# Optimization experiments

Measured on AMD Instinct MI355X. Metric: run time of the kernel, lower is better.

Reference implementation:

```python
import jax, jax.numpy as jnp
import numpy as np

N_NODES = 100000
N_EDGES = 3200000
FEATURE = 128
HIDDEN = 128
N_LAYERS = 3


def _glorot(key, fan_in, fan_out):
    lim = np.sqrt(6.0 / (fan_in + fan_out)).astype(np.float32)
    return jax.random.uniform(key, (fan_in, fan_out), jnp.float32, -lim, lim)


def setup_inputs() -> dict:
    key = jax.random.key(0)
    ks = jax.random.split(key, 8)
    x = jax.random.normal(ks[0], (N_NODES, FEATURE), jnp.float32)
    edge_index = jax.random.randint(ks[1], (2, N_EDGES), 0, N_NODES, jnp.int64)
    W0 = _glorot(ks[2], FEATURE, HIDDEN)
    W1 = _glorot(ks[3], HIDDEN, HIDDEN)
    W2 = _glorot(ks[4], HIDDEN, HIDDEN)
    b0 = jnp.zeros((HIDDEN,), jnp.float32)
    b1 = jnp.zeros((HIDDEN,), jnp.float32)
    b2 = jnp.zeros((HIDDEN,), jnp.float32)
    return {"x": x, "edge_index": edge_index,
            "W0": W0, "b0": b0, "W1": W1, "b1": b1, "W2": W2, "b2": b2}


def _gcn_conv(x, W, b, src, dst, n):
    # PyG GCNConv: linear -> add self loops -> sym-norm aggregate -> +bias
    h = x @ W  # [N, H]
    loop = jnp.arange(n)
    s = jnp.concatenate([src, loop])  # sources incl. self loops
    d = jnp.concatenate([dst, loop])  # targets incl. self loops
    deg = jax.ops.segment_sum(jnp.ones_like(d, dtype=h.dtype), d, num_segments=n)
    dinv = jnp.where(deg > 0, jax.lax.rsqrt(jnp.maximum(deg, 1.0)), 0.0)
    norm = dinv[s] * dinv[d]  # [E+N]
    out = jax.ops.segment_sum(h[s] * norm[:, None], d, num_segments=n)
    return out + b


def reference(x, edge_index, W0, b0, W1, b1, W2, b2):
    # forward of GCN: (GCNConv -> relu -> dropout[eval=no-op]) x layer
    src, dst = edge_index[0], edge_index[1]
    n = x.shape[0]
    for W, b in ((W0, b0), (W1, b1), (W2, b2)):
        x = jax.nn.relu(_gcn_conv(x, W, b, src, dst, n))
    return x
```

## Files before the change

### kernel.cpp

```cpp
#include <hip/hip_runtime.h>
#include <hip/hip_fp16.h>

#define N_NODES 100000
#define N_EDGES 3200000
#define NBUCKETS 391
#define CHUNK 12500

typedef __attribute__((ext_vector_type(8))) short sh8;
typedef __attribute__((ext_vector_type(4))) float fl4;

__device__ inline void split_bf16(float x, short& hi, short& lo) {
    unsigned u = __float_as_uint(x);
    unsigned r = u + 0x7FFFu + ((u >> 16) & 1u);
    hi = (short)(r >> 16);
    float hif = __uint_as_float(r & 0xFFFF0000u);
    float lof = x - hif;
    unsigned u2 = __float_as_uint(lof);
    lo = (short)((u2 + 0x7FFFu + ((u2 >> 16) & 1u)) >> 16);
}


__global__ __launch_bounds__(512) void k_bzero(int* __restrict__ bucket_cnt) {
    int t = threadIdx.x;
    if (t < NBUCKETS) bucket_cnt[t] = 0;
}

__global__ __launch_bounds__(256) void k_bhist(const int* __restrict__ ei_dst,
                                               int* __restrict__ bucket_cnt) {
    __shared__ int h[NBUCKETS];
    int t = threadIdx.x;
    for (int i = t; i < NBUCKETS; i += 256) h[i] = 0;
    __syncthreads();
    int base = blockIdx.x * CHUNK;
    for (int i = t; i < CHUNK; i += 256)
        atomicAdd(&h[ei_dst[base + i] >> 8], 1);
    __syncthreads();
    for (int i = t; i < NBUCKETS; i += 256)
        if (h[i]) atomicAdd(&bucket_cnt[i], h[i]);
}

__global__ __launch_bounds__(512) void k_bscan(const int* __restrict__ bucket_cnt,
                                               int* __restrict__ bucket_base,
                                               int* __restrict__ bucket_fill) {
    __shared__ int s[512];
    int t = threadIdx.x;
    int v = (t < NBUCKETS) ? bucket_cnt[t] : 0;
    s[t] = v;
    __syncthreads();
    for (int off = 1; off < 512; off <<= 1) {
        int x = (t >= off) ? s[t - off] : 0;
        __syncthreads();
        s[t] += x;
        __syncthreads();
    }
    int ex = s[t] - v;
    if (t < NBUCKETS) { bucket_base[t] = ex; bucket_fill[t] = ex; }
    if (t == NBUCKETS - 1) bucket_base[NBUCKETS] = s[t];
}

__global__ __launch_bounds__(256) void k_bscatter(const int* __restrict__ ei,
                                                  int* __restrict__ bucket_fill,
                                                  unsigned* __restrict__ bpairs) {
    __shared__ int h[NBUCKETS];
    __shared__ int basep[NBUCKETS];
    int t = threadIdx.x;
    const int* dstp = ei + N_EDGES;
    int base = blockIdx.x * CHUNK;

    for (int i = t; i < NBUCKETS; i += 256) h[i] = 0;
    __syncthreads();
    for (int i = t; i < CHUNK; i += 256)
        atomicAdd(&h[dstp[base + i] >> 8], 1);
    __syncthreads();
    for (int i = t; i < NBUCKETS; i += 256) {
        int c = h[i];
        basep[i] = c ? atomicAdd(&bucket_fill[i], c) : 0;
    }
    __syncthreads();
    for (int i = t; i < NBUCKETS; i += 256) h[i] = 0;
    __syncthreads();
    for (int i = t; i < CHUNK; i += 256) {
        int d = dstp[base + i];
        int s = ei[base + i];
        int b = d >> 8;
        int r = atomicAdd(&h[b], 1);
        bpairs[basep[b] + r] = (unsigned)s | ((unsigned)(d & 255) << 17);
    }
}

__global__ __launch_bounds__(256) void k_bbuild(const unsigned* __restrict__ bpairs,
                                                const int* __restrict__ bucket_base,
                                                int* __restrict__ row_ptr,
                                                int* __restrict__ cnt,
                                                float* __restrict__ dinv,
                                                int* __restrict__ csr_src) {
    __shared__ int h[256];
    __shared__ int sc[256];
    int b = blockIdx.x;
    int t = threadIdx.x;
    int e0 = bucket_base[b], e1 = bucket_base[b + 1];

    h[t] = 0;
    __syncthreads();
    for (int i = e0 + t; i < e1; i += 256)
        atomicAdd(&h[bpairs[i] >> 17], 1);
    __syncthreads();
    int v = h[t];
    sc[t] = v;
    __syncthreads();
    for (int off = 1; off < 256; off <<= 1) {
        int x = (t >= off) ? sc[t - off] : 0;
        __syncthreads();
        sc[t] += x;
        __syncthreads();
    }
    int ex = sc[t] - v;
    int node = b * 256 + t;
    if (node < N_NODES) {
        cnt[node] = v;
        dinv[node] = rsqrtf((float)(v + 1));
        row_ptr[node] = e0 + ex;
    }
    __syncthreads();
    h[t] = e0 + ex;
    __syncthreads();
    for (int i = e0 + t; i < e1; i += 256) {
        unsigned p = bpairs[i];
        int pos = atomicAdd(&h[p >> 17], 1);
        csr_src[pos] = (int)(p & 0x1FFFFu);
    }
}


__global__ __launch_bounds__(256) void k_wprep(const float* __restrict__ W0,
                                               const float* __restrict__ W1,
                                               const float* __restrict__ W2,
                                               short* __restrict__ fhi,
                                               short* __restrict__ flo) {
    int idx = blockIdx.x * 256 + threadIdx.x;
    int l = idx >> 14, e = idx & 16383;
    const float* W = (l == 0) ? W0 : (l == 1) ? W1 : W2;
    float w = W[e];
    int k = e >> 7, n = e & 127;
    int ks = k >> 5, q = (k >> 3) & 3, j = k & 7;
    int c = n >> 4, n16 = n & 15;
    int lane = q * 16 + n16;
    int dst = ((l * 32 + ks * 8 + c) * 64 + lane) * 8 + j;
    short hi, lo;
    split_bf16(w, hi, lo);
    fhi[dst] = hi;
    flo[dst] = lo;
}


__global__ __launch_bounds__(256) void k_gemm_mfma(const float* __restrict__ X,
                                                   const short* __restrict__ fhi,
                                                   const short* __restrict__ flo,
                                                   const float* __restrict__ dinv,
                                                   __half* __restrict__ H16,
                                                   int layer) {
    int t = threadIdx.x;
    int wave = t >> 6, lane = t & 63;
    int q = lane >> 4, n16 = lane & 15;
    int row_base = blockIdx.x * 128 + wave * 32;

    const sh8* __restrict__ BH = (const sh8*)(fhi + layer * 16384);
    const sh8* __restrict__ BL = (const sh8*)(flo + layer * 16384);

    fl4 acc[2][8];
#pragma unroll
    for (int r = 0; r < 2; ++r)
#pragma unroll
        for (int c = 0; c < 8; ++c) acc[r][c] = (fl4){0.f, 0.f, 0.f, 0.f};

    long long arow[2];
    {
        int r0 = row_base + n16;       if (r0 > N_NODES - 1) r0 = N_NODES - 1;
        int r1 = row_base + 16 + n16;  if (r1 > N_NODES - 1) r1 = N_NODES - 1;
        arow[0] = r0; arow[1] = r1;
    }

#pragma unroll
    for (int ks = 0; ks < 4; ++ks) {
        sh8 ah[2], al[2];
#pragma unroll
        for (int r = 0; r < 2; ++r) {
            const float* px = X + arow[r] * 128 + ks * 32 + q * 8;
            float4 x0 = *(const float4*)px;
            float4 x1 = *(const float4*)(px + 4);
            float xs[8] = {x0.x, x0.y, x0.z, x0.w, x1.x, x1.y, x1.z, x1.w};
#pragma unroll
            for (int j = 0; j < 8; ++j) {
                short h, l;
                split_bf16(xs[j], h, l);
                ah[r][j] = h;
                al[r][j] = l;
            }
        }
#pragma unroll
        for (int c = 0; c < 8; ++c) {
            sh8 bh = BH[(ks * 8 + c) * 64 + lane];
            sh8 bl = BL[(ks * 8 + c) * 64 + lane];
#pragma unroll
            for (int r = 0; r < 2; ++r) {
                acc[r][c] = __builtin_amdgcn_mfma_f32_16x16x32_bf16(ah[r], bh, acc[r][c], 0, 0, 0);
                acc[r][c] = __builtin_amdgcn_mfma_f32_16x16x32_bf16(al[r], bh, acc[r][c], 0, 0, 0);
                acc[r][c] = __builtin_amdgcn_mfma_f32_16x16x32_bf16(ah[r], bl, acc[r][c], 0, 0, 0);
            }
        }
    }

#pragma unroll
    for (int r = 0; r < 2; ++r)
#pragma unroll
        for (int reg = 0; reg < 4; ++reg) {
            int grow = row_base + r * 16 + q * 4 + reg;
            if (grow < N_NODES) {
                float sc = dinv[grow];
                __half* dst = H16 + (long long)grow * 128 + n16;
#pragma unroll
                for (int c = 0; c < 8; ++c)
                    dst[c * 16] = __float2half(acc[r][c][reg] * sc);
            }
        }
}


__global__ __launch_bounds__(256) void k_gather(const __half2* __restrict__ H2,
                                                const int* __restrict__ csr_src,
                                                const int* __restrict__ row_ptr,
                                                const int* __restrict__ cnt,
                                                const float* __restrict__ dinv,
                                                const float* __restrict__ b,
                                                float* __restrict__ out) {
    int node = blockIdx.x * 4 + (threadIdx.x >> 6);
    int lane = threadIdx.x & 63;
    if (node >= N_NODES) return;

    int start = row_ptr[node];
    int n = cnt[node];

    float2 self_ = __half22float2(H2[node * 64 + lane]);
    float accx = self_.x, accy = self_.y;

    int j = 0;
    for (; j + 8 <= n; j += 8) {
        int s[8];
#pragma unroll
        for (int u = 0; u < 8; ++u) s[u] = csr_src[start + j + u];
        float2 h[8];
#pragma unroll
        for (int u = 0; u < 8; ++u) h[u] = __half22float2(H2[s[u] * 64 + lane]);
#pragma unroll
        for (int u = 0; u < 8; ++u) { accx += h[u].x; accy += h[u].y; }
    }
    for (; j < n; ++j) {
        float2 h = __half22float2(H2[csr_src[start + j] * 64 + lane]);
        accx += h.x; accy += h.y;
    }

    float dd = dinv[node];
    float2 bb = ((const float2*)b)[lane];
    float2 v;
    v.x = fmaxf(fmaf(accx, dd, bb.x), 0.0f);
    v.y = fmaxf(fmaf(accy, dd, bb.y), 0.0f);
    ((float2*)out)[node * 64 + lane] = v;
}


extern "C" void kernel_launch(void* const* d_in, const int* in_sizes, int n_in,
                              void* d_out, int out_size, void* d_ws, size_t ws_size,
                              hipStream_t stream) {
    const float* x  = (const float*)d_in[0];
    const int*   ei = (const int*)d_in[1];
    const float* Wm[3] = {(const float*)d_in[2], (const float*)d_in[4], (const float*)d_in[6]};
    const float* bv[3] = {(const float*)d_in[3], (const float*)d_in[5], (const float*)d_in[7]};
    float* out = (float*)d_out;

    char* w = (char*)d_ws;
    int*      row_ptr     = (int*)(w + 0);
    int*      cnt         = (int*)(w + 400384);
    float*    dinv        = (float*)(w + 800768);
    int*      bucket_cnt  = (int*)(w + 1201152);
    int*      bucket_base = (int*)(w + 1203200);
    int*      bucket_fill = (int*)(w + 1205248);
    unsigned* bpairs      = (unsigned*)(w + 1207296);
    int*      csr_src     = (int*)(w + 14007808);
    short*    fragHi      = (short*)(w + 26808320);
    short*    fragLo      = (short*)(w + 26906624);
    __half*   H16         = (__half*)(w + 27004928);

    k_bzero<<<1, 512, 0, stream>>>(bucket_cnt);
    k_bhist<<<256, 256, 0, stream>>>(ei + N_EDGES, bucket_cnt);
    k_bscan<<<1, 512, 0, stream>>>(bucket_cnt, bucket_base, bucket_fill);
    k_bscatter<<<256, 256, 0, stream>>>(ei, bucket_fill, bpairs);
    k_bbuild<<<NBUCKETS, 256, 0, stream>>>(bpairs, bucket_base, row_ptr, cnt, dinv, csr_src);
    k_wprep<<<192, 256, 0, stream>>>(Wm[0], Wm[1], Wm[2], fragHi, fragLo);

    const float* xin = x;
    for (int l = 0; l < 3; ++l) {
        k_gemm_mfma<<<(N_NODES + 127) / 128, 256, 0, stream>>>(xin, fragHi, fragLo,
                                                               dinv, H16, l);
        k_gather<<<(N_NODES + 3) / 4, 256, 0, stream>>>((const __half2*)H16, csr_src,
                                                        row_ptr, cnt, dinv, bv[l], out);
        xin = out;
    }
}
```

Measured before the change: 650.6 us.

## Stage split-bf16 weights in LDS and prefetch all A rows upfront in GEMM

The MFMA GEMM kernel now copies the layer's hi/lo bf16 weight fragments (64KB) into shared memory once per block and reads them from LDS instead of global memory. All of a thread's X row data is loaded up front and split to bf16 before the MFMA loop, so global loads overlap the weight staging. This adds a barrier and high LDS use, which limits blocks per CU (launch bounds request 2). Register pressure also rises from holding all A fragments.

```diff
diff --git a/kernel.cpp b/kernel.cpp
--- a/kernel.cpp
+++ b/kernel.cpp
@@ -153,62 +153,85 @@
 }
 
 
-__global__ __launch_bounds__(256) void k_gemm_mfma(const float* __restrict__ X,
-                                                   const short* __restrict__ fhi,
-                                                   const short* __restrict__ flo,
-                                                   const float* __restrict__ dinv,
-                                                   __half* __restrict__ H16,
-                                                   int layer) {
+__global__ __launch_bounds__(256, 2) void k_gemm_mfma(const float* __restrict__ X,
+                                                      const short* __restrict__ fhi,
+                                                      const short* __restrict__ flo,
+                                                      const float* __restrict__ dinv,
+                                                      __half* __restrict__ H16,
+                                                      int layer) {
+    __shared__ short Bh[16384];
+    __shared__ short Bl[16384];
+
     int t = threadIdx.x;
     int wave = t >> 6, lane = t & 63;
     int q = lane >> 4, n16 = lane & 15;
     int row_base = blockIdx.x * 128 + wave * 32;
 
-    const sh8* __restrict__ BH = (const sh8*)(fhi + layer * 16384);
-    const sh8* __restrict__ BL = (const sh8*)(flo + layer * 16384);
-
-    fl4 acc[2][8];
+    int r0 = row_base + n16;       if (r0 > N_NODES - 1) r0 = N_NODES - 1;
+    int r1 = row_base + 16 + n16;  if (r1 > N_NODES - 1) r1 = N_NODES - 1;
+    const float* p0 = X + (long long)r0 * 128 + q * 8;
+    const float* p1 = X + (long long)r1 * 128 + q * 8;
+    float4 a[2][4][2];
+#pragma unroll
+    for (int ks = 0; ks < 4; ++ks) {
+        a[0][ks][0] = *(const float4*)(p0 + ks * 32);
+        a[0][ks][1] = *(const float4*)(p0 + ks * 32 + 4);
+        a[1][ks][0] = *(const float4*)(p1 + ks * 32);
+        a[1][ks][1] = *(const float4*)(p1 + ks * 32 + 4);
+    }
+
+    {
+        const float4* sh_ = (const float4*)(fhi + layer * 16384);
+        const float4* sl_ = (const float4*)(flo + layer * 16384);
+        float4* dh = (float4*)Bh;
+        float4* dl = (float4*)Bl;
+#pragma unroll
+        for (int i = 0; i < 8; ++i) {
+            dh[t + i * 256] = sh_[t + i * 256];
+            dl[t + i * 256] = sl_[t + i * 256];
+        }
+    }
+
+    sh8 ah[2][4], al[2][4];
 #pragma unroll
     for (int r = 0; r < 2; ++r)
 #pragma unroll
-        for (int c = 0; c < 8; ++c) acc[r][c] = (fl4){0.f, 0.f, 0.f, 0.f};
-
-    long long arow[2];
-    {
-        int r0 = row_base + n16;       if (r0 > N_NODES - 1) r0 = N_NODES - 1;
-        int r1 = row_base + 16 + n16;  if (r1 > N_NODES - 1) r1 = N_NODES - 1;
-        arow[0] = r0; arow[1] = r1;
-    }
-
-#pragma unroll
-    for (int ks = 0; ks < 4; ++ks) {
-        sh8 ah[2], al[2];
-#pragma unroll
-        for (int r = 0; r < 2; ++r) {
-            const float* px = X + arow[r] * 128 + ks * 32 + q * 8;
-            float4 x0 = *(const float4*)px;
-            float4 x1 = *(const float4*)(px + 4);
-            float xs[8] = {x0.x, x0.y, x0.z, x0.w, x1.x, x1.y, x1.z, x1.w};
+        for (int ks = 0; ks < 4; ++ks) {
+            float xs[8];
+            xs[0] = a[r][ks][0].x; xs[1] = a[r][ks][0].y;
+            xs[2] = a[r][ks][0].z; xs[3] = a[r][ks][0].w;
+            xs[4] = a[r][ks][1].x; xs[5] = a[r][ks][1].y;
+            xs[6] = a[r][ks][1].z; xs[7] = a[r][ks][1].w;
 #pragma unroll
             for (int j = 0; j < 8; ++j) {
                 short h, l;
                 split_bf16(xs[j], h, l);
-                ah[r][j] = h;
-                al[r][j] = l;
+                ah[r][ks][j] = h;
+                al[r][ks][j] = l;
             }
         }
+
+    fl4 acc[2][8];
+#pragma unroll
+    for (int r = 0; r < 2; ++r)
+#pragma unroll
+        for (int c = 0; c < 8; ++c) acc[r][c] = (fl4){0.f, 0.f, 0.f, 0.f};
+
+    __syncthreads();
+
+#pragma unroll
+    for (int ks = 0; ks < 4; ++ks)
 #pragma unroll
         for (int c = 0; c < 8; ++c) {
-            sh8 bh = BH[(ks * 8 + c) * 64 + lane];
-            sh8 bl = BL[(ks * 8 + c) * 64 + lane];
+            sh8 bh = *(const sh8*)&Bh[((ks * 8 + c) * 64 + lane) * 8];
+            sh8 bl = *(const sh8*)&Bl[((ks * 8 + c) * 64 + lane) * 8];
 #pragma unroll
             for (int r = 0; r < 2; ++r) {
-                acc[r][c] = __builtin_amdgcn_mfma_f32_16x16x32_bf16(ah[r], bh, acc[r][c], 0, 0, 0);
-                acc[r][c] = __builtin_amdgcn_mfma_f32_16x16x32_bf16(al[r], bh, acc[r][c], 0, 0, 0);
-                acc[r][c] = __builtin_amdgcn_mfma_f32_16x16x32_bf16(ah[r], bl, acc[r][c], 0, 0, 0);
+                acc[r][c] = __builtin_amdgcn_mfma_f32_16x16x32_bf16(ah[r][ks], bh, acc[r][c], 0, 0, 0);
+                acc[r][c] = __builtin_amdgcn_mfma_f32_16x16x32_bf16(al[r][ks], bh, acc[r][c], 0, 0, 0);
+                acc[r][c] = __builtin_amdgcn_mfma_f32_16x16x32_bf16(ah[r][ks], bl, acc[r][c], 0, 0, 0);
             }
         }
-    }
 
 #pragma unroll
     for (int r = 0; r < 2; ++r)
```

Result: faster. 625.8 us (-3.8%).

## Shrink GEMM tile to 16 rows per wave, preload inputs, double CSR-build chunk count

Applied to the files above, without the earlier changes.

The MFMA GEMM now has each wave handle a single 16-row tile instead of two. It preloads all four K-slices of X up front and batches the B-fragment loads per K-step. Launch bounds request 3 blocks per SM, and the grid grows to 1563 blocks, aiming for more waves in flight and better latency hiding at the cost of reusing each B fragment across fewer rows. The CSR bucket histogram and scatter now use 512 chunks of 6250 edges for more parallelism. The gather kernel makes the wave index uniform via readfirstlane.

```diff
diff --git a/kernel.cpp b/kernel.cpp
--- a/kernel.cpp
+++ b/kernel.cpp
@@ -4,7 +4,8 @@
 #define N_NODES 100000
 #define N_EDGES 3200000
 #define NBUCKETS 391
-#define CHUNK 12500
+#define NCHUNKB 512
+#define CHUNK 6250
 
 typedef __attribute__((ext_vector_type(8))) short sh8;
 typedef __attribute__((ext_vector_type(4))) float fl4;
@@ -153,76 +154,76 @@
 }
 
 
-__global__ __launch_bounds__(256) void k_gemm_mfma(const float* __restrict__ X,
-                                                   const short* __restrict__ fhi,
-                                                   const short* __restrict__ flo,
-                                                   const float* __restrict__ dinv,
-                                                   __half* __restrict__ H16,
-                                                   int layer) {
+__global__ __launch_bounds__(256, 3) void k_gemm_mfma(const float* __restrict__ X,
+                                                      const short* __restrict__ fhi,
+                                                      const short* __restrict__ flo,
+                                                      const float* __restrict__ dinv,
+                                                      __half* __restrict__ H16) {
     int t = threadIdx.x;
     int wave = t >> 6, lane = t & 63;
     int q = lane >> 4, n16 = lane & 15;
-    int row_base = blockIdx.x * 128 + wave * 32;
-
-    const sh8* __restrict__ BH = (const sh8*)(fhi + layer * 16384);
-    const sh8* __restrict__ BL = (const sh8*)(flo + layer * 16384);
-
-    fl4 acc[2][8];
-#pragma unroll
-    for (int r = 0; r < 2; ++r)
-#pragma unroll
-        for (int c = 0; c < 8; ++c) acc[r][c] = (fl4){0.f, 0.f, 0.f, 0.f};
-
-    long long arow[2];
-    {
-        int r0 = row_base + n16;       if (r0 > N_NODES - 1) r0 = N_NODES - 1;
-        int r1 = row_base + 16 + n16;  if (r1 > N_NODES - 1) r1 = N_NODES - 1;
-        arow[0] = r0; arow[1] = r1;
-    }
-
+    int tile = blockIdx.x * 4 + wave;
+    int row_base = tile * 16;
+
+    int r0 = row_base + n16;
+    if (r0 > N_NODES - 1) r0 = N_NODES - 1;
+    const float* p0 = X + (long long)r0 * 128 + q * 8;
+    float4 a[4][2];
 #pragma unroll
     for (int ks = 0; ks < 4; ++ks) {
-        sh8 ah[2], al[2];
-#pragma unroll
-        for (int r = 0; r < 2; ++r) {
-            const float* px = X + arow[r] * 128 + ks * 32 + q * 8;
-            float4 x0 = *(const float4*)px;
-            float4 x1 = *(const float4*)(px + 4);
-            float xs[8] = {x0.x, x0.y, x0.z, x0.w, x1.x, x1.y, x1.z, x1.w};
-#pragma unroll
-            for (int j = 0; j < 8; ++j) {
-                short h, l;
-                split_bf16(xs[j], h, l);
-                ah[r][j] = h;
-                al[r][j] = l;
-            }
+        a[ks][0] = *(const float4*)(p0 + ks * 32);
+        a[ks][1] = *(const float4*)(p0 + ks * 32 + 4);
+    }
+
+    sh8 ah[4], al[4];
+#pragma unroll
+    for (int ks = 0; ks < 4; ++ks) {
+        float xs[8];
+        xs[0] = a[ks][0].x; xs[1] = a[ks][0].y; xs[2] = a[ks][0].z; xs[3] = a[ks][0].w;
+        xs[4] = a[ks][1].x; xs[5] = a[ks][1].y; xs[6] = a[ks][1].z; xs[7] = a[ks][1].w;
+#pragma unroll
+        for (int j = 0; j < 8; ++j) {
+            short h, l;
+            split_bf16(xs[j], h, l);
+            ah[ks][j] = h;
+            al[ks][j] = l;
         }
+    }
+
+    const sh8* __restrict__ BH = (const sh8*)fhi;
+    const sh8* __restrict__ BL = (const sh8*)flo;
+
+    fl4 acc[8];
+#pragma unroll
+    for (int c = 0; c < 8; ++c) acc[c] = (fl4){0.f, 0.f, 0.f, 0.f};
+
+#pragma unroll
+    for (int ks = 0; ks < 4; ++ks) {
+        sh8 bh[8], bl[8];
 #pragma unroll
         for (int c = 0; c < 8; ++c) {
-            sh8 bh = BH[(ks * 8 + c) * 64 + lane];
-            sh8 bl = BL[(ks * 8 + c) * 64 + lane];
-#pragma unroll
-            for (int r = 0; r < 2; ++r) {
-                acc[r][c] = __builtin_amdgcn_mfma_f32_16x16x32_bf16(ah[r], bh, acc[r][c], 0, 0, 0);
-                acc[r][c] = __builtin_amdgcn_mfma_f32_16x16x32_bf16(al[r], bh, acc[r][c], 0, 0, 0);
-                acc[r][c] = __builtin_amdgcn_mfma_f32_16x16x32_bf16(ah[r], bl, acc[r][c], 0, 0, 0);
-            }
+            bh[c] = BH[(ks * 8 + c) * 64 + lane];
+            bl[c] = BL[(ks * 8 + c) * 64 + lane];
         }
-    }
-
-#pragma unroll
-    for (int r = 0; r < 2; ++r)
-#pragma unroll
-        for (int reg = 0; reg < 4; ++reg) {
-            int grow = row_base + r * 16 + q * 4 + reg;
-            if (grow < N_NODES) {
-                float sc = dinv[grow];
-                __half* dst = H16 + (long long)grow * 128 + n16;
-#pragma unroll
-                for (int c = 0; c < 8; ++c)
-                    dst[c * 16] = __float2half(acc[r][c][reg] * sc);
-            }
+#pragma unroll
+        for (int c = 0; c < 8; ++c) {
+            acc[c] = __builtin_amdgcn_mfma_f32_16x16x32_bf16(ah[ks], bh[c], acc[c], 0, 0, 0);
+            acc[c] = __builtin_amdgcn_mfma_f32_16x16x32_bf16(al[ks], bh[c], acc[c], 0, 0, 0);
+            acc[c] = __builtin_amdgcn_mfma_f32_16x16x32_bf16(ah[ks], bl[c], acc[c], 0, 0, 0);
         }
+    }
+
+#pragma unroll
+    for (int reg = 0; reg < 4; ++reg) {
+        int grow = row_base + q * 4 + reg;
+        if (grow < N_NODES) {
+            float sc = dinv[grow];
+            __half* dst = H16 + (long long)grow * 128 + n16;
+#pragma unroll
+            for (int c = 0; c < 8; ++c)
+                dst[c * 16] = __float2half(acc[c][reg] * sc);
+        }
+    }
 }
 
 
@@ -233,7 +234,8 @@
                                                 const float* __restrict__ dinv,
                                                 const float* __restrict__ b,
                                                 float* __restrict__ out) {
-    int node = blockIdx.x * 4 + (threadIdx.x >> 6);
+    int wv = __builtin_amdgcn_readfirstlane(threadIdx.x >> 6);
+    int node = blockIdx.x * 4 + wv;
     int lane = threadIdx.x & 63;
     if (node >= N_NODES) return;
 
@@ -291,16 +293,16 @@
     __half*   H16         = (__half*)(w + 27004928);
 
     k_bzero<<<1, 512, 0, stream>>>(bucket_cnt);
-    k_bhist<<<256, 256, 0, stream>>>(ei + N_EDGES, bucket_cnt);
+    k_bhist<<<NCHUNKB, 256, 0, stream>>>(ei + N_EDGES, bucket_cnt);
     k_bscan<<<1, 512, 0, stream>>>(bucket_cnt, bucket_base, bucket_fill);
-    k_bscatter<<<256, 256, 0, stream>>>(ei, bucket_fill, bpairs);
+    k_bscatter<<<NCHUNKB, 256, 0, stream>>>(ei, bucket_fill, bpairs);
     k_bbuild<<<NBUCKETS, 256, 0, stream>>>(bpairs, bucket_base, row_ptr, cnt, dinv, csr_src);
     k_wprep<<<192, 256, 0, stream>>>(Wm[0], Wm[1], Wm[2], fragHi, fragLo);
 
     const float* xin = x;
     for (int l = 0; l < 3; ++l) {
-        k_gemm_mfma<<<(N_NODES + 127) / 128, 256, 0, stream>>>(xin, fragHi, fragLo,
-                                                               dinv, H16, l);
+        k_gemm_mfma<<<1563, 256, 0, stream>>>(xin, fragHi + l * 16384, fragLo + l * 16384,
+                                              dinv, H16);
         k_gather<<<(N_NODES + 3) / 4, 256, 0, stream>>>((const __half2*)H16, csr_src,
                                                         row_ptr, cnt, dinv, bv[l], out);
         xin = out;
```

Result: faster. 624.8 us (-4.0%).
